# Optimization experiments

Measured on AMD Instinct MI355X. Metric: run time of the kernel, lower is better.

Reference implementation:

```python
import jax, jax.numpy as jnp
import numpy as np

B, P, D, TOK = 128, 197, 768, 512
K, TOPK, L, H = 16, 8, 2, 12
EPS = 0.05
LN_EPS = 1e-5


def _layer_norm(x, w, b):
    m = jnp.mean(x, axis=-1, keepdims=True)
    v = jnp.var(x, axis=-1, keepdims=True)
    return (x - m) * jax.lax.rsqrt(v + LN_EPS) * w + b


def _attn(x, qw, qb, kvw, kvb, pw, pb):
    b, n, d = x.shape
    hd = d // H
    q = (x @ qw + qb).reshape(b, n, H, hd)
    kv = (x @ kvw + kvb).reshape(b, n, 2, H, hd)
    k, v = kv[:, :, 0], kv[:, :, 1]
    att = jnp.einsum('bnhd,bmhd->bnmh', q, k) * (hd ** -0.5)
    att = jax.nn.softmax(att, axis=2)
    out = jnp.einsum('bnmh,bmhd->bnhd', att, v).reshape(b, n, d)
    return out @ pw + pb


def _forward(img_feature_proj, img_patch_feats, templates,
             ln1_w, ln1_b, q_w, q_b, kv_w, kv_b, proj_w, proj_b,
             ln2_w, ln2_b, fc1_w, fc1_b, fc2_w, fc2_b, att_fc_w, att_fc_b):
    bs = img_patch_feats.shape[0]
    tpl = jnp.broadcast_to(templates, (bs, K, D))
    x = jnp.concatenate([tpl, img_patch_feats], axis=1)  # [B, K+P, D]
    for i in range(L):  # pre-LN ClipCap-style transformer
        x = x + _attn(_layer_norm(x, ln1_w[i], ln1_b[i]), q_w[i], q_b[i], kv_w[i], kv_b[i], proj_w[i], proj_b[i])
        h = _layer_norm(x, ln2_w[i], ln2_b[i])
        x = x + jax.nn.relu(h @ fc1_w[i] + fc1_b[i]) @ fc2_w[i] + fc2_b[i]
    lat = jax.nn.sigmoid(x[:, :K, :] @ att_fc_w + att_fc_b)  # [B, K, TOK]
    aw = jax.nn.softmax(jnp.einsum('bkt,bt->bk', lat, img_feature_proj), axis=1)  # [B, K]
    sorted_idx = jnp.argsort(-aw, axis=1)[:, :TOPK]  # descending, truncated
    counts = jnp.sum(aw > EPS, axis=1)  # over all K, like torch.nonzero(mask)
    num_r = jnp.clip(counts, 1, TOPK)  # [B]
    # vectorized per-sample compaction: first num_r indices sorted ascending, rest keep order
    j = jnp.arange(TOPK)[None, :]
    keys = jnp.where(j < num_r[:, None], sorted_idx, K + j)
    perm = jnp.argsort(keys, axis=1)
    select_id = jnp.take_along_axis(sorted_idx, perm, axis=1)  # [B, TOPK]
    sel = jnp.take_along_axis(lat, select_id[:, :, None], axis=1)  # [B, TOPK, TOK]
    norm = jnp.linalg.norm(sel, axis=-1, keepdims=True)
    sel = sel / jnp.maximum(norm, 1e-12)
    return sel, num_r


def setup_inputs():
    key = jax.random.key(0)
    ks = jax.random.split(key, 10)
    s = 0.02
    f = jnp.float32
    return {
        'img_feature_proj': jax.random.normal(ks[0], (B, TOK), f),
        'img_patch_feats': jax.random.normal(ks[1], (B, P, D), f),
        'templates': jax.random.normal(ks[2], (1, K, D), f),
        'ln1_w': jnp.ones((L, D), f), 'ln1_b': jnp.zeros((L, D), f),
        'q_w': jax.random.normal(ks[3], (L, D, D), f) * s, 'q_b': jnp.zeros((L, D), f),
        'kv_w': jax.random.normal(ks[4], (L, D, 2 * D), f) * s, 'kv_b': jnp.zeros((L, 2 * D), f),
        'proj_w': jax.random.normal(ks[5], (L, D, D), f) * s, 'proj_b': jnp.zeros((L, D), f),
        'ln2_w': jnp.ones((L, D), f), 'ln2_b': jnp.zeros((L, D), f),
        'fc1_w': jax.random.normal(ks[6], (L, D, 2 * D), f) * s, 'fc1_b': jnp.zeros((L, 2 * D), f),
        'fc2_w': jax.random.normal(ks[7], (L, 2 * D, D), f) * s, 'fc2_b': jnp.zeros((L, D), f),
        'att_fc_w': jax.random.normal(ks[8], (D, TOK), f) * s, 'att_fc_b': jnp.zeros((TOK,), f),
    }


def reference(img_feature_proj, img_patch_feats, templates,
              ln1_w, ln1_b, q_w, q_b, kv_w, kv_b, proj_w, proj_b,
              ln2_w, ln2_b, fc1_w, fc1_b, fc2_w, fc2_b, att_fc_w, att_fc_b):
    return _forward(img_feature_proj, img_patch_feats, templates,
                    ln1_w, ln1_b, q_w, q_b, kv_w, kv_b, proj_w, proj_b,
                    ln2_w, ln2_b, fc1_w, fc1_b, fc2_w, fc2_b, att_fc_w, att_fc_b)
```

## Files before the change

kernel.cpp:

```cpp
#include <hip/hip_runtime.h>
#include <math.h>

#define B_    128
#define P_    197
#define D_    768
#define TOK_  512
#define K_    16
#define TOPK_ 8
#define L_    2
#define H_    12
#define HD_   64
#define NTOK  213
#define MROWS (B_ * NTOK)

typedef _Float16 f16;
typedef __attribute__((ext_vector_type(8))) _Float16 f16x8;
typedef __attribute__((ext_vector_type(4))) _Float16 f16x4;
typedef __attribute__((ext_vector_type(4))) float f32x4;

__device__ __forceinline__ void gload_lds16(const void* g, void* l) {
  __builtin_amdgcn_global_load_lds(
      (const __attribute__((address_space(1))) unsigned int*)g,
      (__attribute__((address_space(3))) unsigned int*)l, 16, 0, 0);
}

__device__ __forceinline__ float wred_sum(float v) {
#pragma unroll
  for (int o = 32; o > 0; o >>= 1) v += __shfl_xor(v, o);
  return v;
}
__device__ __forceinline__ float wred_max(float v) {
#pragma unroll
  for (int o = 32; o > 0; o >>= 1) v = fmaxf(v, __shfl_xor(v, o));
  return v;
}
__device__ __forceinline__ float red16_max(float v) {
#pragma unroll
  for (int o = 8; o > 0; o >>= 1) v = fmaxf(v, __shfl_xor(v, o));
  return v;
}
__device__ __forceinline__ float red16_sum(float v) {
#pragma unroll
  for (int o = 8; o > 0; o >>= 1) v += __shfl_xor(v, o);
  return v;
}

__global__ __launch_bounds__(256) void concat_kernel(
    const float* __restrict__ tpl, const float* __restrict__ patches,
    float* __restrict__ x) {
  size_t i = (size_t)blockIdx.x * 256 + threadIdx.x;
  const size_t total = (size_t)MROWS * (D_ / 4);
  if (i >= total) return;
  size_t row = i / (D_ / 4);
  int c = (int)(i % (D_ / 4)) * 4;
  size_t b = row / NTOK;
  int n = (int)(row % NTOK);
  float4 v;
  if (n < K_) v = *(const float4*)(tpl + (size_t)n * D_ + c);
  else        v = *(const float4*)(patches + ((size_t)b * P_ + (n - K_)) * D_ + c);
  *(float4*)(x + row * D_ + c) = v;
}

__global__ __launch_bounds__(64) void ln_split_kernel(
    const float* __restrict__ x, const float* __restrict__ w,
    const float* __restrict__ b, f16* __restrict__ yh, f16* __restrict__ yl) {
  size_t row = blockIdx.x;
  int lane = threadIdx.x;
  const float* xr = x + row * D_;
  float4 v[3];
#pragma unroll
  for (int j = 0; j < 3; ++j) v[j] = *(const float4*)(xr + j * 256 + lane * 4);
  float s = 0.f, sq = 0.f;
#pragma unroll
  for (int j = 0; j < 3; ++j) {
    s += v[j].x + v[j].y + v[j].z + v[j].w;
    sq = fmaf(v[j].x, v[j].x, sq); sq = fmaf(v[j].y, v[j].y, sq);
    sq = fmaf(v[j].z, v[j].z, sq); sq = fmaf(v[j].w, v[j].w, sq);
  }
#pragma unroll
  for (int o = 32; o > 0; o >>= 1) { s += __shfl_xor(s, o); sq += __shfl_xor(sq, o); }
  float mean = s * (1.f / D_);
  float var = sq * (1.f / D_) - mean * mean;
  float rs = rsqrtf(var + 1e-5f);
#pragma unroll
  for (int j = 0; j < 3; ++j) {
    int col = j * 256 + lane * 4;
    float4 wv = *(const float4*)(w + col);
    float4 bv = *(const float4*)(b + col);
    float o0 = (v[j].x - mean) * rs * wv.x + bv.x;
    float o1 = (v[j].y - mean) * rs * wv.y + bv.y;
    float o2 = (v[j].z - mean) * rs * wv.z + bv.z;
    float o3 = (v[j].w - mean) * rs * wv.w + bv.w;
    f16x4 hi = {(f16)o0, (f16)o1, (f16)o2, (f16)o3};
    f16x4 lo = {(f16)(o0 - (float)hi[0]), (f16)(o1 - (float)hi[1]),
                (f16)(o2 - (float)hi[2]), (f16)(o3 - (float)hi[3])};
    *(f16x4*)&yh[row * D_ + col] = hi;
    *(f16x4*)&yl[row * D_ + col] = lo;
  }
}

__global__ __launch_bounds__(256) void transpose_split(
    const float* __restrict__ W, f16* __restrict__ Wh, f16* __restrict__ Wl,
    int Kd, int Nd) {
  __shared__ float t[32][33];
  const int n0 = blockIdx.x * 32, k0 = blockIdx.y * 32;
  const int tx = threadIdx.x & 31, ty = threadIdx.x >> 5;
#pragma unroll
  for (int j = 0; j < 4; ++j)
    t[ty + 8 * j][tx] = W[(size_t)(k0 + ty + 8 * j) * Nd + n0 + tx];
  __syncthreads();
#pragma unroll
  for (int j = 0; j < 4; ++j) {
    float v = t[tx][ty + 8 * j];
    f16 hi = (f16)v;
    size_t off = (size_t)(n0 + ty + 8 * j) * Kd + k0 + tx;
    Wh[off] = hi;
    Wl[off] = (f16)(v - (float)hi);
  }
}

template <int ACT, bool RESID, bool OUTSPLIT>
__global__ __launch_bounds__(256) void gemm_split(
    const f16* __restrict__ Ah, const f16* __restrict__ Al,
    const f16* __restrict__ Wh, const f16* __restrict__ Wl,
    const float* __restrict__ bias, float* __restrict__ Cf,
    f16* __restrict__ Ch, f16* __restrict__ Cl, int M, int N, int K) {
  __shared__ __align__(16) f16 S[2][4][128][32];
  const int tid = threadIdx.x;
  const int bm = blockIdx.x * 128, bn = blockIdx.y * 128;
  const int w = tid >> 6, lane = tid & 63;
  const int wm = (w & 1) * 64, wn = (w >> 1) * 64;
  const int fr = lane & 15, kg = lane >> 4;
  f32x4 acc[4][4];
  const f32x4 z = {0.f, 0.f, 0.f, 0.f};
#pragma unroll
  for (int i = 0; i < 4; ++i)
#pragma unroll
    for (int j = 0; j < 4; ++j) acc[i][j] = z;
  const int srow = tid >> 2;
  const int c_l  = (tid & 3) ^ ((tid >> 3) & 3);
  const int cswz = (kg ^ ((fr >> 1) & 3)) * 8;

  auto STAGE = [&](int k0, int buf) {
#pragma unroll
    for (int j = 0; j < 2; ++j) {
      int arow = bm + j * 64 + srow; if (arow >= M) arow = M - 1;
      int brow = bn + j * 64 + srow;
      size_t aoff = (size_t)arow * K + k0 + c_l * 8;
      size_t boff = (size_t)brow * K + k0 + c_l * 8;
      char* base = (char*)&S[buf][0][0][0] + j * 4096 + w * 1024;
      gload_lds16(Ah + aoff, base);
      gload_lds16(Al + aoff, base + 8192);
      gload_lds16(Wh + boff, base + 16384);
      gload_lds16(Wl + boff, base + 24576);
    }
  };
  auto COMPUTE = [&](int buf) {
    f16x8 ah[4], al[4], bh[4], bl[4];
#pragma unroll
    for (int i = 0; i < 4; ++i) {
      ah[i] = *(const f16x8*)&S[buf][0][wm + i * 16 + fr][cswz];
      al[i] = *(const f16x8*)&S[buf][1][wm + i * 16 + fr][cswz];
      bh[i] = *(const f16x8*)&S[buf][2][wn + i * 16 + fr][cswz];
      bl[i] = *(const f16x8*)&S[buf][3][wn + i * 16 + fr][cswz];
    }
#pragma unroll
    for (int i = 0; i < 4; ++i)
#pragma unroll
      for (int j = 0; j < 4; ++j) {
        acc[i][j] = __builtin_amdgcn_mfma_f32_16x16x32_f16(ah[i], bh[j], acc[i][j], 0, 0, 0);
        acc[i][j] = __builtin_amdgcn_mfma_f32_16x16x32_f16(ah[i], bl[j], acc[i][j], 0, 0, 0);
        acc[i][j] = __builtin_amdgcn_mfma_f32_16x16x32_f16(al[i], bh[j], acc[i][j], 0, 0, 0);
      }
  };

  const int nt = K / 32;
  int cur = 0;
  STAGE(0, 0);
  for (int t = 0; t < nt - 1; ++t) {
    STAGE((t + 1) * 32, cur ^ 1);
    asm volatile("s_waitcnt vmcnt(8)" ::: "memory");
    __builtin_amdgcn_s_barrier();
    __builtin_amdgcn_sched_barrier(0);
    COMPUTE(cur);
    __builtin_amdgcn_s_barrier();
    cur ^= 1;
  }
  asm volatile("s_waitcnt vmcnt(0)" ::: "memory");
  __builtin_amdgcn_s_barrier();
  __builtin_amdgcn_sched_barrier(0);
  COMPUTE(cur);

#pragma unroll
  for (int j = 0; j < 4; ++j) {
    const int gc = bn + wn + j * 16 + fr;
    const float bv = bias[gc];
#pragma unroll
    for (int i = 0; i < 4; ++i) {
#pragma unroll
      for (int rg = 0; rg < 4; ++rg) {
        int gr = bm + wm + i * 16 + kg * 4 + rg;
        if (gr < M) {
          float val = acc[i][j][rg] + bv;
          if (ACT == 1) val = fmaxf(val, 0.f);
          if (ACT == 2) val = 1.f / (1.f + expf(-val));
          size_t off = (size_t)gr * N + gc;
          if (OUTSPLIT) {
            f16 hi = (f16)val;
            Ch[off] = hi;
            Cl[off] = (f16)(val - (float)hi);
          } else {
            if (RESID) val += Cf[off];
            Cf[off] = val;
          }
        }
      }
    }
  }
}

__global__ __launch_bounds__(256) void attn_mfma(
    const f16* __restrict__ Qh, const f16* __restrict__ Ql,
    const f16* __restrict__ KVh, const f16* __restrict__ KVl,
    f16* __restrict__ Oh, f16* __restrict__ Ol) {
  __shared__ __align__(16) f16 Ksh[64][64];
  __shared__ __align__(16) f16 Ksl[64][64];
  __shared__ __align__(16) f16 Vsh[64][64];
  __shared__ __align__(16) f16 Vsl[64][64];
  __shared__ __align__(16) f16 Psh[4][32][64];
  __shared__ __align__(16) f16 Psl[4][32][64];
  const int b = blockIdx.x, h = blockIdx.y, zb = blockIdx.z;
  const int tid = threadIdx.x, w = tid >> 6, lane = tid & 63;
  const int fr = lane & 15, kg = lane >> 4;
  const int qbase = zb * 128 + w * 32;
  const size_t rowbase = (size_t)b * NTOK;
  const int hoff = h * HD_;
  const f32x4 z4 = {0.f, 0.f, 0.f, 0.f};

  f16x8 qfh[2][2], qfl[2][2];
#pragma unroll
  for (int mf = 0; mf < 2; ++mf) {
    int qr = qbase + mf * 16 + fr; if (qr >= NTOK) qr = NTOK - 1;
    const size_t ro = (rowbase + qr) * D_ + hoff;
#pragma unroll
    for (int ks = 0; ks < 2; ++ks) {
      qfh[mf][ks] = *(const f16x8*)&Qh[ro + ks * 32 + kg * 8];
      qfl[mf][ks] = *(const f16x8*)&Ql[ro + ks * 32 + kg * 8];
    }
  }

  f32x4 oacc[2][4];
#pragma unroll
  for (int mf = 0; mf < 2; ++mf)
#pragma unroll
    for (int df = 0; df < 4; ++df) oacc[mf][df] = z4;
  float m_r[2][4], l_r[2][4];
#pragma unroll
  for (int mf = 0; mf < 2; ++mf)
#pragma unroll
    for (int rg = 0; rg < 4; ++rg) { m_r[mf][rg] = -INFINITY; l_r[mf][rg] = 0.f; }

  for (int t = 0; t < 4; ++t) {
    const int t0 = t * 64;
    __syncthreads();
#pragma unroll
    for (int s = 0; s < 2; ++s) {
      int slot = tid + s * 256;
      int trow = slot >> 3, pch = slot & 7;
      int lch = pch ^ (trow & 7);
      int tok = t0 + trow; if (tok >= NTOK) tok = NTOK - 1;
      size_t src = (rowbase + tok) * (size_t)(2 * D_) + hoff + lch * 8;
      gload_lds16(KVh + src, (char*)&Ksh[0][0] + s * 4096 + w * 1024);
      gload_lds16(KVl + src, (char*)&Ksl[0][0] + s * 4096 + w * 1024);
    }
    {
      int tloc = tid & 63, dg = tid >> 6;
      int tok = t0 + tloc; if (tok >= NTOK) tok = NTOK - 1;
      size_t src = (rowbase + tok) * (size_t)(2 * D_) + D_ + hoff + dg * 16;
      f16x8 v0h = *(const f16x8*)&KVh[src];
      f16x8 v1h = *(const f16x8*)&KVh[src + 8];
      f16x8 v0l = *(const f16x8*)&KVl[src];
      f16x8 v1l = *(const f16x8*)&KVl[src + 8];
      int ch = tloc >> 3, pos = tloc & 7;
#pragma unroll
      for (int i = 0; i < 8; ++i) {
        int d0 = dg * 16 + i, d1 = d0 + 8;
        Vsh[d0][((ch ^ (d0 & 7)) << 3) | pos] = v0h[i];
        Vsh[d1][((ch ^ (d1 & 7)) << 3) | pos] = v1h[i];
        Vsl[d0][((ch ^ (d0 & 7)) << 3) | pos] = v0l[i];
        Vsl[d1][((ch ^ (d1 & 7)) << 3) | pos] = v1l[i];
      }
    }
    __syncthreads();
    f16x8 kbh[4][2], kbl[4][2];
#pragma unroll
    for (int nf = 0; nf < 4; ++nf)
#pragma unroll
      for (int ks = 0; ks < 2; ++ks) {
        int phys = (((ks * 4 + kg) ^ (fr & 7))) * 8;
        kbh[nf][ks] = *(const f16x8*)&Ksh[nf * 16 + fr][phys];
        kbl[nf][ks] = *(const f16x8*)&Ksl[nf * 16 + fr][phys];
      }
    f32x4 sacc[2][4];
#pragma unroll
    for (int mf = 0; mf < 2; ++mf)
#pragma unroll
      for (int nf = 0; nf < 4; ++nf) sacc[mf][nf] = z4;
#pragma unroll
    for (int ks = 0; ks < 2; ++ks)
#pragma unroll
      for (int mf = 0; mf < 2; ++mf)
#pragma unroll
        for (int nf = 0; nf < 4; ++nf) {
          sacc[mf][nf] = __builtin_amdgcn_mfma_f32_16x16x32_f16(qfh[mf][ks], kbh[nf][ks], sacc[mf][nf], 0, 0, 0);
          sacc[mf][nf] = __builtin_amdgcn_mfma_f32_16x16x32_f16(qfh[mf][ks], kbl[nf][ks], sacc[mf][nf], 0, 0, 0);
          sacc[mf][nf] = __builtin_amdgcn_mfma_f32_16x16x32_f16(qfl[mf][ks], kbh[nf][ks], sacc[mf][nf], 0, 0, 0);
        }
#pragma unroll
    for (int nf = 0; nf < 4; ++nf) {
      bool valid = (t0 + nf * 16 + fr) < NTOK;
#pragma unroll
      for (int mf = 0; mf < 2; ++mf)
#pragma unroll
        for (int rg = 0; rg < 4; ++rg)
          sacc[mf][nf][rg] = valid ? sacc[mf][nf][rg] * 0.125f : -INFINITY;
    }
#pragma unroll
    for (int mf = 0; mf < 2; ++mf) {
      float scl[4];
#pragma unroll
      for (int rg = 0; rg < 4; ++rg) {
        float mx = fmaxf(fmaxf(sacc[mf][0][rg], sacc[mf][1][rg]),
                         fmaxf(sacc[mf][2][rg], sacc[mf][3][rg]));
        mx = red16_max(mx);
        float nm = fmaxf(m_r[mf][rg], mx);
        scl[rg] = __expf(m_r[mf][rg] - nm);
        m_r[mf][rg] = nm;
        float ts = 0.f;
        int qlc = mf * 16 + kg * 4 + rg;
#pragma unroll
        for (int nf = 0; nf < 4; ++nf) {
          float p = __expf(sacc[mf][nf][rg] - nm);
          ts += p;
          f16 ph = (f16)p;
          int tl = nf * 16 + fr;
          int off = (((tl >> 3) ^ (qlc & 7)) << 3) | (tl & 7);
          Psh[w][qlc][off] = ph;
          Psl[w][qlc][off] = (f16)(p - (float)ph);
        }
        ts = red16_sum(ts);
        l_r[mf][rg] = l_r[mf][rg] * scl[rg] + ts;
      }
#pragma unroll
      for (int df = 0; df < 4; ++df)
#pragma unroll
        for (int rg = 0; rg < 4; ++rg)
          oacc[mf][df][rg] *= scl[rg];
    }
    f16x8 vbh[4][2], vbl[4][2];
#pragma unroll
    for (int df = 0; df < 4; ++df)
#pragma unroll
      for (int ks = 0; ks < 2; ++ks) {
        int phys = (((ks * 4 + kg) ^ (fr & 7))) * 8;
        vbh[df][ks] = *(const f16x8*)&Vsh[df * 16 + fr][phys];
        vbl[df][ks] = *(const f16x8*)&Vsl[df * 16 + fr][phys];
      }
    f16x8 pah[2][2], pal[2][2];
#pragma unroll
    for (int mf = 0; mf < 2; ++mf)
#pragma unroll
      for (int ks = 0; ks < 2; ++ks) {
        int phys = (((ks * 4 + kg) ^ (fr & 7))) * 8;
        pah[mf][ks] = *(const f16x8*)&Psh[w][mf * 16 + fr][phys];
        pal[mf][ks] = *(const f16x8*)&Psl[w][mf * 16 + fr][phys];
      }
#pragma unroll
    for (int ks = 0; ks < 2; ++ks)
#pragma unroll
      for (int mf = 0; mf < 2; ++mf)
#pragma unroll
        for (int df = 0; df < 4; ++df) {
          oacc[mf][df] = __builtin_amdgcn_mfma_f32_16x16x32_f16(pah[mf][ks], vbh[df][ks], oacc[mf][df], 0, 0, 0);
          oacc[mf][df] = __builtin_amdgcn_mfma_f32_16x16x32_f16(pah[mf][ks], vbl[df][ks], oacc[mf][df], 0, 0, 0);
          oacc[mf][df] = __builtin_amdgcn_mfma_f32_16x16x32_f16(pal[mf][ks], vbh[df][ks], oacc[mf][df], 0, 0, 0);
        }
  }
#pragma unroll
  for (int mf = 0; mf < 2; ++mf)
#pragma unroll
    for (int rg = 0; rg < 4; ++rg) {
      int qr = qbase + mf * 16 + kg * 4 + rg;
      if (qr < NTOK) {
        float inv = 1.f / l_r[mf][rg];
        size_t ro = (rowbase + qr) * D_ + hoff;
#pragma unroll
        for (int df = 0; df < 4; ++df) {
          float val = oacc[mf][df][rg] * inv;
          f16 hi = (f16)val;
          Oh[ro + df * 16 + fr] = hi;
          Ol[ro + df * 16 + fr] = (f16)(val - (float)hi);
        }
      }
    }
}

__global__ __launch_bounds__(256) void gather_split(
    const float* __restrict__ x, f16* __restrict__ oh, f16* __restrict__ ol) {
  int idx = blockIdx.x * 256 + threadIdx.x;
  if (idx >= B_ * K_ * (D_ / 4)) return;
  int row = idx / (D_ / 4);
  int c4 = (idx % (D_ / 4)) * 4;
  int b = row >> 4, k = row & 15;
  const float* src = x + ((size_t)(b * NTOK + k)) * D_ + c4;
  f16x4 hi, lo;
#pragma unroll
  for (int i = 0; i < 4; ++i) {
    float v = src[i];
    hi[i] = (f16)v;
    lo[i] = (f16)(v - (float)hi[i]);
  }
  *(f16x4*)&oh[(size_t)row * D_ + c4] = hi;
  *(f16x4*)&ol[(size_t)row * D_ + c4] = lo;
}

__global__ __launch_bounds__(64) void logits_kernel(
    const float* __restrict__ lat, const float* __restrict__ proj,
    float* __restrict__ logits) {
  int bk = blockIdx.x;
  int b = bk >> 4;
  int lane = threadIdx.x;
  const float* lr = lat + (size_t)bk * TOK_;
  const float* pr = proj + (size_t)b * TOK_;
  float s = 0.f;
#pragma unroll
  for (int i = 0; i < 8; ++i) s = fmaf(lr[lane + 64 * i], pr[lane + 64 * i], s);
  s = wred_sum(s);
  if (lane == 0) logits[bk] = s;
}

__global__ __launch_bounds__(64) void select_kernel(
    const float* __restrict__ logits, const float* __restrict__ lat,
    float* __restrict__ out_sel, float* __restrict__ out_numr) {
  const int b = blockIdx.x;
  const int lane = threadIdx.x;
  __shared__ float aw_s[16];
  __shared__ int sel_id_s[8];
  __shared__ int numr_s;
  float v = (lane < 16) ? logits[b * 16 + lane] : -INFINITY;
  float mx = wred_max(v);
  float e = (lane < 16) ? expf(v - mx) : 0.f;
  float sum = wred_sum(e);
  float aw = e / sum;
  if (lane < 16) aw_s[lane] = aw;
  unsigned long long ball = __ballot(lane < 16 && aw > 0.05f);
  int counts = __popcll(ball);
  __syncthreads();
  if (lane == 0) {
    int num_r = counts < 1 ? 1 : (counts > TOPK_ ? TOPK_ : counts);
    numr_s = num_r;
    bool used[16];
#pragma unroll
    for (int i = 0; i < 16; ++i) used[i] = false;
    int sorted_idx[8];
    for (int j = 0; j < 8; ++j) {
      float bv = -INFINITY; int bi = 0;
      for (int i = 0; i < 16; ++i)
        if (!used[i] && aw_s[i] > bv) { bv = aw_s[i]; bi = i; }
      used[bi] = true;
      sorted_idx[j] = bi;
    }
    int keys[8];
    for (int j = 0; j < 8; ++j) keys[j] = (j < num_r) ? sorted_idx[j] : (16 + j);
    bool kused[8];
    for (int j = 0; j < 8; ++j) kused[j] = false;
    for (int slot = 0; slot < 8; ++slot) {
      int bk = 1 << 30, bj = 0;
      for (int j = 0; j < 8; ++j)
        if (!kused[j] && keys[j] < bk) { bk = keys[j]; bj = j; }
      kused[bj] = true;
      sel_id_s[slot] = sorted_idx[bj];
    }
  }
  __syncthreads();
  for (int j = 0; j < 8; ++j) {
    int id = sel_id_s[j];
    const float* row = lat + ((size_t)b * 16 + id) * TOK_;
    float vals[8];
    float sq = 0.f;
#pragma unroll
    for (int i = 0; i < 8; ++i) {
      vals[i] = row[lane + 64 * i];
      sq = fmaf(vals[i], vals[i], sq);
    }
    sq = wred_sum(sq);
    float inv = 1.f / fmaxf(sqrtf(sq), 1e-12f);
#pragma unroll
    for (int i = 0; i < 8; ++i)
      out_sel[((size_t)b * 8 + j) * TOK_ + lane + 64 * i] = vals[i] * inv;
  }
  if (lane == 0) out_numr[b] = (float)numr_s;
}

extern "C" void kernel_launch(void* const* d_in, const int* in_sizes, int n_in,
                              void* d_out, int out_size, void* d_ws, size_t ws_size,
                              hipStream_t stream) {
  const float* img_feature_proj = (const float*)d_in[0];
  const float* img_patch_feats  = (const float*)d_in[1];
  const float* templates        = (const float*)d_in[2];
  const float* ln1_w  = (const float*)d_in[3];
  const float* ln1_b  = (const float*)d_in[4];
  const float* q_w    = (const float*)d_in[5];
  const float* q_b    = (const float*)d_in[6];
  const float* kv_w   = (const float*)d_in[7];
  const float* kv_b   = (const float*)d_in[8];
  const float* proj_w = (const float*)d_in[9];
  const float* proj_b = (const float*)d_in[10];
  const float* ln2_w  = (const float*)d_in[11];
  const float* ln2_b  = (const float*)d_in[12];
  const float* fc1_w  = (const float*)d_in[13];
  const float* fc1_b  = (const float*)d_in[14];
  const float* fc2_w  = (const float*)d_in[15];
  const float* fc2_b  = (const float*)d_in[16];
  const float* att_fc_w = (const float*)d_in[17];
  const float* att_fc_b = (const float*)d_in[18];

  char* ws = (char*)d_ws;
  const size_t XB = (size_t)MROWS * D_ * 4;
  float* x_f = (float*)ws;  ws += XB;
  auto alloc_f16 = [&](size_t n) { f16* p = (f16*)ws; ws += n * 2; return p; };
  f16* wq_h  = alloc_f16((size_t)768 * 768);
  f16* wq_l  = alloc_f16((size_t)768 * 768);
  f16* wkv_h = alloc_f16((size_t)1536 * 768);
  f16* wkv_l = alloc_f16((size_t)1536 * 768);
  f16* wp_h  = alloc_f16((size_t)768 * 768);
  f16* wp_l  = alloc_f16((size_t)768 * 768);
  f16* wf1_h = alloc_f16((size_t)1536 * 768);
  f16* wf1_l = alloc_f16((size_t)1536 * 768);
  f16* wf2_h = alloc_f16((size_t)768 * 1536);
  f16* wf2_l = alloc_f16((size_t)768 * 1536);
  f16* awt_h = alloc_f16((size_t)512 * 768);
  f16* awt_l = alloc_f16((size_t)512 * 768);
  f16* lat_h = alloc_f16((size_t)2048 * 768);
  f16* lat_l = alloc_f16((size_t)2048 * 768);
  float* lat    = (float*)ws; ws += (size_t)2048 * 512 * 4;
  float* logits = (float*)ws; ws += 8192;
  const size_t fixed_bytes = (size_t)(ws - (char*)d_ws);

  int NB = B_;
  while (NB > 1) {
    size_t CHE = (size_t)NB * NTOK * D_;
    if (fixed_bytes + 16 * CHE <= ws_size) break;
    NB >>= 1;
  }
  const size_t CHE = (size_t)NB * NTOK * D_;
  f16* h_h = (f16*)ws;
  f16* h_l = h_h + CHE;
  f16* qh  = h_l + CHE;
  f16* ql  = qh + CHE;
  f16* kvh = ql + CHE;
  f16* kvl = kvh + 2 * CHE;
  f16* fc1o_h = qh;
  f16* fc1o_l = kvh;

  {
    size_t total = (size_t)MROWS * (D_ / 4);
    concat_kernel<<<(unsigned)((total + 255) / 256), 256, 0, stream>>>(
        templates, img_patch_feats, x_f);
  }
  transpose_split<<<dim3(16, 24), 256, 0, stream>>>(att_fc_w, awt_h, awt_l, 768, 512);

  const int nchunks = B_ / NB;
  for (int l = 0; l < L_; ++l) {
    transpose_split<<<dim3(24, 24), 256, 0, stream>>>(q_w + (size_t)l * 768 * 768, wq_h, wq_l, 768, 768);
    transpose_split<<<dim3(48, 24), 256, 0, stream>>>(kv_w + (size_t)l * 768 * 1536, wkv_h, wkv_l, 768, 1536);
    transpose_split<<<dim3(24, 24), 256, 0, stream>>>(proj_w + (size_t)l * 768 * 768, wp_h, wp_l, 768, 768);
    transpose_split<<<dim3(48, 24), 256, 0, stream>>>(fc1_w + (size_t)l * 768 * 1536, wf1_h, wf1_l, 768, 1536);
    transpose_split<<<dim3(24, 48), 256, 0, stream>>>(fc2_w + (size_t)l * 1536 * 768, wf2_h, wf2_l, 1536, 768);
    for (int c = 0; c < nchunks; ++c) {
      const int b0 = c * NB;
      const int Rc = NB * NTOK;
      const int mt = (Rc + 127) / 128;
      float* xc = x_f + (size_t)b0 * NTOK * D_;
      ln_split_kernel<<<Rc, 64, 0, stream>>>(xc, ln1_w + l * D_, ln1_b + l * D_, h_h, h_l);
      gemm_split<0, false, true><<<dim3(mt, 6), 256, 0, stream>>>(
          h_h, h_l, wq_h, wq_l, q_b + l * D_, nullptr, qh, ql, Rc, 768, 768);
      gemm_split<0, false, true><<<dim3(mt, 12), 256, 0, stream>>>(
          h_h, h_l, wkv_h, wkv_l, kv_b + l * 1536, nullptr, kvh, kvl, Rc, 1536, 768);
      attn_mfma<<<dim3(NB, H_, 2), 256, 0, stream>>>(qh, ql, kvh, kvl, h_h, h_l);
      gemm_split<0, true, false><<<dim3(mt, 6), 256, 0, stream>>>(
          h_h, h_l, wp_h, wp_l, proj_b + l * D_, xc, nullptr, nullptr, Rc, 768, 768);
      ln_split_kernel<<<Rc, 64, 0, stream>>>(xc, ln2_w + l * D_, ln2_b + l * D_, h_h, h_l);
      gemm_split<1, false, true><<<dim3(mt, 12), 256, 0, stream>>>(
          h_h, h_l, wf1_h, wf1_l, fc1_b + l * 1536, nullptr, fc1o_h, fc1o_l, Rc, 1536, 768);
      gemm_split<0, true, false><<<dim3(mt, 6), 256, 0, stream>>>(
          fc1o_h, fc1o_l, wf2_h, wf2_l, fc2_b + l * D_, xc, nullptr, nullptr, Rc, 768, 1536);
    }
  }

  gather_split<<<(B_ * K_ * (D_ / 4) + 255) / 256, 256, 0, stream>>>(x_f, lat_h, lat_l);
  gemm_split<2, false, false><<<dim3(16, 4), 256, 0, stream>>>(
      lat_h, lat_l, awt_h, awt_l, att_fc_b, lat, nullptr, nullptr, B_ * K_, TOK_, 768);

  logits_kernel<<<B_ * K_, 64, 0, stream>>>(lat, img_feature_proj, logits);
  select_kernel<<<B_, 64, 0, stream>>>(logits, lat, (float*)d_out,
                                       (float*)d_out + (size_t)B_ * TOPK_ * TOK_);
}
```

Measured before the change: 3.024 ms.

## Fuse Q and KV projections into one QKV GEMM and swap grid order

Q and KV weights are packed into a single transposed 2304-wide weight buffer with a combined bias, so the QKV projection runs as one GEMM instead of two. The attention kernel now reads Q, K and V from that interleaved buffer using the wider row stride. The GEMM grid is also transposed so consecutive blocks share the same M tile across N tiles, which should improve L2 reuse of the A operand. The intent is to cut a launch and reread the LN output once rather than twice. The cost is a larger per-chunk scratch buffer, which may lower the chunk size chosen to fit the workspace.

```diff
diff --git a/kernel.cpp b/kernel.cpp
--- a/kernel.cpp
+++ b/kernel.cpp
@@ -12,6 +12,7 @@
 #define HD_   64
 #define NTOK  213
 #define MROWS (B_ * NTOK)
+#define QKVN  2304
 
 typedef _Float16 f16;
 typedef __attribute__((ext_vector_type(8))) _Float16 f16x8;
@@ -119,6 +120,13 @@
   }
 }
 
+__global__ __launch_bounds__(256) void combine_bias(
+    const float* __restrict__ qb, const float* __restrict__ kvb,
+    float* __restrict__ out) {
+  int i = blockIdx.x * 256 + threadIdx.x;
+  if (i < QKVN) out[i] = (i < D_) ? qb[i] : kvb[i - D_];
+}
+
 template <int ACT, bool RESID, bool OUTSPLIT>
 __global__ __launch_bounds__(256) void gemm_split(
     const f16* __restrict__ Ah, const f16* __restrict__ Al,
@@ -127,7 +135,7 @@
     f16* __restrict__ Ch, f16* __restrict__ Cl, int M, int N, int K) {
   __shared__ __align__(16) f16 S[2][4][128][32];
   const int tid = threadIdx.x;
-  const int bm = blockIdx.x * 128, bn = blockIdx.y * 128;
+  const int bn = blockIdx.x * 128, bm = blockIdx.y * 128;
   const int w = tid >> 6, lane = tid & 63;
   const int wm = (w & 1) * 64, wn = (w >> 1) * 64;
   const int fr = lane & 15, kg = lane >> 4;
@@ -220,8 +228,7 @@
 }
 
 __global__ __launch_bounds__(256) void attn_mfma(
-    const f16* __restrict__ Qh, const f16* __restrict__ Ql,
-    const f16* __restrict__ KVh, const f16* __restrict__ KVl,
+    const f16* __restrict__ QKVh, const f16* __restrict__ QKVl,
     f16* __restrict__ Oh, f16* __restrict__ Ol) {
   __shared__ __align__(16) f16 Ksh[64][64];
   __shared__ __align__(16) f16 Ksl[64][64];
@@ -241,11 +248,11 @@
 #pragma unroll
   for (int mf = 0; mf < 2; ++mf) {
     int qr = qbase + mf * 16 + fr; if (qr >= NTOK) qr = NTOK - 1;
-    const size_t ro = (rowbase + qr) * D_ + hoff;
+    const size_t ro = (rowbase + qr) * QKVN + hoff;
 #pragma unroll
     for (int ks = 0; ks < 2; ++ks) {
-      qfh[mf][ks] = *(const f16x8*)&Qh[ro + ks * 32 + kg * 8];
-      qfl[mf][ks] = *(const f16x8*)&Ql[ro + ks * 32 + kg * 8];
+      qfh[mf][ks] = *(const f16x8*)&QKVh[ro + ks * 32 + kg * 8];
+      qfl[mf][ks] = *(const f16x8*)&QKVl[ro + ks * 32 + kg * 8];
     }
   }
 
@@ -269,18 +276,18 @@
       int trow = slot >> 3, pch = slot & 7;
       int lch = pch ^ (trow & 7);
       int tok = t0 + trow; if (tok >= NTOK) tok = NTOK - 1;
-      size_t src = (rowbase + tok) * (size_t)(2 * D_) + hoff + lch * 8;
-      gload_lds16(KVh + src, (char*)&Ksh[0][0] + s * 4096 + w * 1024);
-      gload_lds16(KVl + src, (char*)&Ksl[0][0] + s * 4096 + w * 1024);
+      size_t src = (rowbase + tok) * (size_t)QKVN + D_ + hoff + lch * 8;
+      gload_lds16(QKVh + src, (char*)&Ksh[0][0] + s * 4096 + w * 1024);
+      gload_lds16(QKVl + src, (char*)&Ksl[0][0] + s * 4096 + w * 1024);
     }
     {
       int tloc = tid & 63, dg = tid >> 6;
       int tok = t0 + tloc; if (tok >= NTOK) tok = NTOK - 1;
-      size_t src = (rowbase + tok) * (size_t)(2 * D_) + D_ + hoff + dg * 16;
-      f16x8 v0h = *(const f16x8*)&KVh[src];
-      f16x8 v1h = *(const f16x8*)&KVh[src + 8];
-      f16x8 v0l = *(const f16x8*)&KVl[src];
-      f16x8 v1l = *(const f16x8*)&KVl[src + 8];
+      size_t src = (rowbase + tok) * (size_t)QKVN + 2 * D_ + hoff + dg * 16;
+      f16x8 v0h = *(const f16x8*)&QKVh[src];
+      f16x8 v1h = *(const f16x8*)&QKVh[src + 8];
+      f16x8 v0l = *(const f16x8*)&QKVl[src];
+      f16x8 v1l = *(const f16x8*)&QKVl[src + 8];
       int ch = tloc >> 3, pos = tloc & 7;
 #pragma unroll
       for (int i = 0; i < 8; ++i) {
@@ -529,20 +536,19 @@
   const size_t XB = (size_t)MROWS * D_ * 4;
   float* x_f = (float*)ws;  ws += XB;
   auto alloc_f16 = [&](size_t n) { f16* p = (f16*)ws; ws += n * 2; return p; };
-  f16* wq_h  = alloc_f16((size_t)768 * 768);
-  f16* wq_l  = alloc_f16((size_t)768 * 768);
-  f16* wkv_h = alloc_f16((size_t)1536 * 768);
-  f16* wkv_l = alloc_f16((size_t)1536 * 768);
-  f16* wp_h  = alloc_f16((size_t)768 * 768);
-  f16* wp_l  = alloc_f16((size_t)768 * 768);
-  f16* wf1_h = alloc_f16((size_t)1536 * 768);
-  f16* wf1_l = alloc_f16((size_t)1536 * 768);
-  f16* wf2_h = alloc_f16((size_t)768 * 1536);
-  f16* wf2_l = alloc_f16((size_t)768 * 1536);
-  f16* awt_h = alloc_f16((size_t)512 * 768);
-  f16* awt_l = alloc_f16((size_t)512 * 768);
-  f16* lat_h = alloc_f16((size_t)2048 * 768);
-  f16* lat_l = alloc_f16((size_t)2048 * 768);
+  f16* wqkv_h = alloc_f16((size_t)QKVN * 768);
+  f16* wqkv_l = alloc_f16((size_t)QKVN * 768);
+  f16* wp_h   = alloc_f16((size_t)768 * 768);
+  f16* wp_l   = alloc_f16((size_t)768 * 768);
+  f16* wf1_h  = alloc_f16((size_t)1536 * 768);
+  f16* wf1_l  = alloc_f16((size_t)1536 * 768);
+  f16* wf2_h  = alloc_f16((size_t)768 * 1536);
+  f16* wf2_l  = alloc_f16((size_t)768 * 1536);
+  f16* awt_h  = alloc_f16((size_t)512 * 768);
+  f16* awt_l  = alloc_f16((size_t)512 * 768);
+  f16* lat_h  = alloc_f16((size_t)2048 * 768);
+  f16* lat_l  = alloc_f16((size_t)2048 * 768);
+  float* qkv_b  = (float*)ws; ws += QKVN * 4;
   float* lat    = (float*)ws; ws += (size_t)2048 * 512 * 4;
   float* logits = (float*)ws; ws += 8192;
   const size_t fixed_bytes = (size_t)(ws - (char*)d_ws);
@@ -554,14 +560,12 @@
     NB >>= 1;
   }
   const size_t CHE = (size_t)NB * NTOK * D_;
-  f16* h_h = (f16*)ws;
-  f16* h_l = h_h + CHE;
-  f16* qh  = h_l + CHE;
-  f16* ql  = qh + CHE;
-  f16* kvh = ql + CHE;
-  f16* kvl = kvh + 2 * CHE;
-  f16* fc1o_h = qh;
-  f16* fc1o_l = kvh;
+  f16* h_h   = (f16*)ws;
+  f16* h_l   = h_h + CHE;
+  f16* qkvh  = h_l + CHE;
+  f16* qkvl  = qkvh + 3 * CHE;
+  f16* fc1o_h = qkvh;
+  f16* fc1o_l = qkvl;
 
   {
     size_t total = (size_t)MROWS * (D_ / 4);
@@ -572,8 +576,10 @@
 
   const int nchunks = B_ / NB;
   for (int l = 0; l < L_; ++l) {
-    transpose_split<<<dim3(24, 24), 256, 0, stream>>>(q_w + (size_t)l * 768 * 768, wq_h, wq_l, 768, 768);
-    transpose_split<<<dim3(48, 24), 256, 0, stream>>>(kv_w + (size_t)l * 768 * 1536, wkv_h, wkv_l, 768, 1536);
+    transpose_split<<<dim3(24, 24), 256, 0, stream>>>(q_w + (size_t)l * 768 * 768, wqkv_h, wqkv_l, 768, 768);
+    transpose_split<<<dim3(48, 24), 256, 0, stream>>>(kv_w + (size_t)l * 768 * 1536,
+        wqkv_h + (size_t)768 * 768, wqkv_l + (size_t)768 * 768, 768, 1536);
+    combine_bias<<<(QKVN + 255) / 256, 256, 0, stream>>>(q_b + l * D_, kv_b + l * 1536, qkv_b);
     transpose_split<<<dim3(24, 24), 256, 0, stream>>>(proj_w + (size_t)l * 768 * 768, wp_h, wp_l, 768, 768);
     transpose_split<<<dim3(48, 24), 256, 0, stream>>>(fc1_w + (size_t)l * 768 * 1536, wf1_h, wf1_l, 768, 1536);
     transpose_split<<<dim3(24, 48), 256, 0, stream>>>(fc2_w + (size_t)l * 1536 * 768, wf2_h, wf2_l, 1536, 768);
@@ -583,23 +589,21 @@
       const int mt = (Rc + 127) / 128;
       float* xc = x_f + (size_t)b0 * NTOK * D_;
       ln_split_kernel<<<Rc, 64, 0, stream>>>(xc, ln1_w + l * D_, ln1_b + l * D_, h_h, h_l);
-      gemm_split<0, false, true><<<dim3(mt, 6), 256, 0, stream>>>(
-          h_h, h_l, wq_h, wq_l, q_b + l * D_, nullptr, qh, ql, Rc, 768, 768);
-      gemm_split<0, false, true><<<dim3(mt, 12), 256, 0, stream>>>(
-          h_h, h_l, wkv_h, wkv_l, kv_b + l * 1536, nullptr, kvh, kvl, Rc, 1536, 768);
-      attn_mfma<<<dim3(NB, H_, 2), 256, 0, stream>>>(qh, ql, kvh, kvl, h_h, h_l);
-      gemm_split<0, true, false><<<dim3(mt, 6), 256, 0, stream>>>(
+      gemm_split<0, false, true><<<dim3(QKVN / 128, mt), 256, 0, stream>>>(
+          h_h, h_l, wqkv_h, wqkv_l, qkv_b, nullptr, qkvh, qkvl, Rc, QKVN, 768);
+      attn_mfma<<<dim3(NB, H_, 2), 256, 0, stream>>>(qkvh, qkvl, h_h, h_l);
+      gemm_split<0, true, false><<<dim3(6, mt), 256, 0, stream>>>(
           h_h, h_l, wp_h, wp_l, proj_b + l * D_, xc, nullptr, nullptr, Rc, 768, 768);
       ln_split_kernel<<<Rc, 64, 0, stream>>>(xc, ln2_w + l * D_, ln2_b + l * D_, h_h, h_l);
-      gemm_split<1, false, true><<<dim3(mt, 12), 256, 0, stream>>>(
+      gemm_split<1, false, true><<<dim3(12, mt), 256, 0, stream>>>(
           h_h, h_l, wf1_h, wf1_l, fc1_b + l * 1536, nullptr, fc1o_h, fc1o_l, Rc, 1536, 768);
-      gemm_split<0, true, false><<<dim3(mt, 6), 256, 0, stream>>>(
+      gemm_split<0, true, false><<<dim3(6, mt), 256, 0, stream>>>(
           fc1o_h, fc1o_l, wf2_h, wf2_l, fc2_b + l * D_, xc, nullptr, nullptr, Rc, 768, 1536);
     }
   }
 
   gather_split<<<(B_ * K_ * (D_ / 4) + 255) / 256, 256, 0, stream>>>(x_f, lat_h, lat_l);
-  gemm_split<2, false, false><<<dim3(16, 4), 256, 0, stream>>>(
+  gemm_split<2, false, false><<<dim3(4, 16), 256, 0, stream>>>(
       lat_h, lat_l, awt_h, awt_l, att_fc_b, lat, nullptr, nullptr, B_ * K_, TOK_, 768);
 
   logits_kernel<<<B_ * K_, 64, 0, stream>>>(lat, img_feature_proj, logits);
```

After: 2.820 ms. 1.07x faster.
